# Optimization experiments

Measured on AMD Instinct MI355X. Metric: run time of the kernel, lower is better.

The kernel has to match this reference:

```python
import jax, jax.numpy as jnp
import numpy as np


def setup_inputs() -> dict:
    key = jax.random.key(0)
    k1, k2 = jax.random.split(key)
    B, D = 16384, 256
    return {
        "outputs": jax.random.normal(k1, (B, D), dtype=jnp.float32),
        "targets": jax.random.normal(k2, (B, D), dtype=jnp.float32),
    }


def reference(outputs, targets):
    # Cosine-similarity logits: (o @ t^T) / (||o||_row * ||t||_col)
    logits = outputs @ targets.T                      # [B, B]
    o_norm = jnp.linalg.norm(outputs, axis=1)         # [B]
    t_norm = jnp.linalg.norm(targets, axis=1)         # [B]
    logits = logits / o_norm[:, None] / t_norm[None, :]
    # Cross-entropy with labels = arange(B): mean over rows of (logsumexp - diag logit)
    logZ = jax.nn.logsumexp(logits, axis=1)           # [B]
    diag = jnp.diagonal(logits)                       # [B]
    loss = jnp.mean(logZ - diag)
    return loss
```

## Files before the change

kernel.cpp:

```cpp
#include <hip/hip_runtime.h>
#include <hip/hip_bf16.h>
#include <stdint.h>

#define BROWS 16384
#define DIM   256
#define BM    128
#define NBM   (BROWS / BM)
#define NBNR  16
#define NSTG  8
#define NCHUNK 32

#define LOG2E 1.44269504088896340736f

typedef __attribute__((ext_vector_type(8))) int  i32x8;
typedef __attribute__((ext_vector_type(4))) float f32x4;
typedef __attribute__((ext_vector_type(2))) float f32x2;
typedef unsigned char uchar;

#if __has_builtin(__builtin_amdgcn_exp2f)
#define EXP2(x) __builtin_amdgcn_exp2f(x)
#else
#define EXP2(x) exp2f(x)
#endif

__device__ __forceinline__ void gload_lds16(const void* g, void* l) {
  __builtin_amdgcn_global_load_lds(
      (const __attribute__((address_space(1))) void*)g,
      (__attribute__((address_space(3))) void*)l, 16, 0, 0);
}

__device__ __forceinline__ unsigned q4(float x) {
  float a = fabsf(x);
  unsigned q = (a >= 0.25f) + (a >= 0.75f) + (a >= 1.25f) + (a >= 1.75f) +
               (a >= 2.5f) + (a >= 3.5f) + (a >= 5.0f);
  return q | ((__float_as_uint(x) >> 28) & 8u);
}


__global__ void normalize_both(const float* __restrict__ o,
                               const float* __restrict__ t,
                               uchar* __restrict__ o4,
                               uchar* __restrict__ t4,
                               float* __restrict__ dlog) {
  int row  = blockIdx.x * 4 + (threadIdx.x >> 6);
  int lane = threadIdx.x & 63;
  float4 a = *(reinterpret_cast<const float4*>(o + (size_t)row * DIM) + lane);
  float4 b = *(reinterpret_cast<const float4*>(t + (size_t)row * DIM) + lane);
  float sso = a.x * a.x + a.y * a.y + a.z * a.z + a.w * a.w;
  float sst = b.x * b.x + b.y * b.y + b.z * b.z + b.w * b.w;
  float d   = a.x * b.x + a.y * b.y + a.z * b.z + a.w * b.w;
#pragma unroll
  for (int m = 1; m < 64; m <<= 1) {
    sso += __shfl_xor(sso, m);
    sst += __shfl_xor(sst, m);
    d   += __shfl_xor(d, m);
  }
  float ro = rsqrtf(sso);
  float rt = rsqrtf(sst);
  if (lane == 0) dlog[row] = d * ro * rt;
  float qo = ro * (16.0f * LOG2E);
  float qt = rt * 16.0f;
  unsigned wo = q4(a.x * qo) | (q4(a.y * qo) << 4) |
                (q4(a.z * qo) << 8) | (q4(a.w * qo) << 12);
  unsigned wt = q4(b.x * qt) | (q4(b.y * qt) << 4) |
                (q4(b.z * qt) << 8) | (q4(b.w * qt) << 12);
  size_t taddr = (size_t)(row >> 4) * 2048 + (size_t)((lane >> 3) * 256) +
                 (size_t)((row & 15) * 16) + (size_t)((lane & 7) * 2);
  *reinterpret_cast<unsigned short*>(o4 + taddr) = (unsigned short)wo;
  *reinterpret_cast<unsigned short*>(t4 + taddr) = (unsigned short)wt;
}

__global__ __launch_bounds__(512, 8) void gemm_expsum(
    const uchar* __restrict__ A4,
    const uchar* __restrict__ B4,
    float* __restrict__ partial) {
  __shared__ __align__(16) uchar Bs[2][16384];

  int b   = blockIdx.x;
  int xcd = b & 7;
  int idx = b >> 3;
  int bm  = xcd * 16 + (idx & 15);
  int bnr = idx >> 4;

  int tid  = threadIdx.x;
  int lane = tid & 63;
  int wid  = tid >> 6;
  int wr   = wid & 3;
  int wch  = wid >> 2;

  const uchar* Ap = A4 + (size_t)(bm * 8 + wr * 2) * 2048 + (size_t)lane * 16;
  const uchar* Bg = B4 + (size_t)bnr * 131072;

  i32x8 af[2][2];
#pragma unroll
  for (int m = 0; m < 2; ++m)
#pragma unroll
    for (int kt = 0; kt < 2; ++kt) {
      int4 d = *reinterpret_cast<const int4*>(Ap + m * 2048 + kt * 1024);
      af[m][kt] = (i32x8){d.x, d.y, d.z, d.w, 0, 0, 0, 0};
    }

  f32x2 v2[4];
#pragma unroll
  for (int j = 0; j < 4; ++j) v2[j] = (f32x2){0.f, 0.f};

  const f32x4 zero4 = {0.f, 0.f, 0.f, 0.f};
  i32x8 b0 = (i32x8){0, 0, 0, 0, 0, 0, 0, 0};
  i32x8 b1 = (i32x8){0, 0, 0, 0, 0, 0, 0, 0};

#define STAGE(st, s)                                                           \
  {                                                                            \
    _Pragma("unroll") for (int p = 0; p < 2; ++p)                              \
        gload_lds16(Bg + (size_t)(st) * 16384 + p * 8192 + wid * 1024 +        \
                        lane * 16,                                             \
                    (char*)Bs[s] + p * 8192 + wid * 1024 + lane * 16);         \
  }

#define COMPUTE(s)                                                             \
  {                                                                            \
    const uchar* bb = Bs[s];                                                   \
    _Pragma("unroll") for (int nn = 0; nn < 4; ++nn) {                         \
      const uchar* cb = bb + (wch * 4 + nn) * 2048 + lane * 16;                \
      *reinterpret_cast<int4*>(&b0) = *reinterpret_cast<const int4*>(cb);      \
      *reinterpret_cast<int4*>(&b1) = *reinterpret_cast<const int4*>(cb + 1024); \
      f32x4 a0 = __builtin_amdgcn_mfma_scale_f32_16x16x128_f8f6f4(             \
          af[0][0], b0, zero4, 4, 4, 0, 0x7B7B7B7B, 0, 0x7B7B7B7B);            \
      f32x4 a1 = __builtin_amdgcn_mfma_scale_f32_16x16x128_f8f6f4(             \
          af[1][0], b0, zero4, 4, 4, 0, 0x7B7B7B7B, 0, 0x7B7B7B7B);            \
      a0 = __builtin_amdgcn_mfma_scale_f32_16x16x128_f8f6f4(                   \
          af[0][1], b1, a0, 4, 4, 0, 0x7B7B7B7B, 0, 0x7B7B7B7B);               \
      a1 = __builtin_amdgcn_mfma_scale_f32_16x16x128_f8f6f4(                   \
          af[1][1], b1, a1, 4, 4, 0, 0x7B7B7B7B, 0, 0x7B7B7B7B);               \
      v2[0] += (f32x2){EXP2(a0[0]), EXP2(a0[1])};                              \
      v2[1] += (f32x2){EXP2(a0[2]), EXP2(a0[3])};                              \
      v2[2] += (f32x2){EXP2(a1[0]), EXP2(a1[1])};                              \
      v2[3] += (f32x2){EXP2(a1[2]), EXP2(a1[3])};                              \
    }                                                                          \
  }

  STAGE(0, 0);
  __syncthreads();
#pragma unroll
  for (int st = 0; st < NSTG; ++st) {
    if (st < NSTG - 1) STAGE(st + 1, (st + 1) & 1);
    COMPUTE(st & 1);
    if (st < NSTG - 1) __syncthreads();
  }
#undef STAGE
#undef COMPUTE

  float v[8];
#pragma unroll
  for (int j = 0; j < 8; ++j) v[j] = v2[j >> 1][j & 1];
#pragma unroll
  for (int s = 0; s < 3; ++s) {
    const int len = 8 >> s;
    const int bit = (lane >> s) & 1;
#pragma unroll
    for (int t = 0; t < 4; ++t) {
      if (t < (len >> 1)) {
        float a = v[2 * t], b2 = v[2 * t + 1];
        float recv = __shfl_xor(bit ? a : b2, 1 << s);
        v[t] = (bit ? b2 : a) + recv;
      }
    }
  }
  v[0] += __shfl_xor(v[0], 8);
  if ((lane & 8) == 0) {
    int j   = lane & 7;
    int sub = lane >> 4;
    int row = bm * BM + wr * 32 + (j >> 2) * 16 + sub * 4 + (j & 3);
    partial[(size_t)row * NCHUNK + ((bnr << 1) | wch)] = v[0];
  }
}

__global__ void row_finish(const float* __restrict__ partial,
                           const float* __restrict__ dlog,
                           float* __restrict__ rowloss) {
  int row = blockIdx.x * 256 + threadIdx.x;
  const float4* p = reinterpret_cast<const float4*>(partial + (size_t)row * NCHUNK);
  float s = 0.f;
#pragma unroll
  for (int q = 0; q < 8; ++q) {
    float4 pq = p[q];
    s += (pq.x + pq.y) + (pq.z + pq.w);
  }
  rowloss[row] = logf(s) - dlog[row];
}

__global__ void final_reduce(const float* __restrict__ rl, float* __restrict__ out) {
  __shared__ float sm[16];
  float s = 0.f;
  for (int i = threadIdx.x; i < BROWS; i += 1024) s += rl[i];
#pragma unroll
  for (int m = 1; m < 64; m <<= 1) s += __shfl_xor(s, m);
  int wid = threadIdx.x >> 6, lane = threadIdx.x & 63;
  if (lane == 0) sm[wid] = s;
  __syncthreads();
  if (wid == 0) {
    float v = (lane < 16) ? sm[lane] : 0.f;
#pragma unroll
    for (int m = 1; m < 16; m <<= 1) v += __shfl_xor(v, m);
    if (lane == 0) out[0] = v / (float)BROWS;
  }
}

extern "C" void kernel_launch(void* const* d_in, const int* in_sizes, int n_in,
                              void* d_out, int out_size, void* d_ws, size_t ws_size,
                              hipStream_t stream) {
  const float* outputs = (const float*)d_in[0];
  const float* targets = (const float*)d_in[1];
  float* out = (float*)d_out;
  char* ws = (char*)d_ws;

  uchar* o4      = (uchar*)ws;
  uchar* t4      = (uchar*)(ws + (size_t)2 * 1024 * 1024);
  float* partial = (float*)(ws + (size_t)4 * 1024 * 1024);
  float* dlog    = (float*)(ws + (size_t)6 * 1024 * 1024);
  float* rowloss = (float*)(ws + (size_t)6 * 1024 * 1024 + 65536);

  normalize_both<<<BROWS / 4, 256, 0, stream>>>(outputs, targets, o4, t4, dlog);
  gemm_expsum<<<NBM * NBNR, 512, 0, stream>>>(o4, t4, partial);
  row_finish<<<BROWS / 256, 256, 0, stream>>>(partial, dlog, rowloss);
  final_reduce<<<1, 1024, 0, stream>>>(rowloss, out);
}
```

Baseline: 63.16 us.

## Switch FP4 GEMM to 32x32x64 scaled MFMA with matching operand layout

Replaces the 16x16x128 FP4 scaled MFMA tiles with 32x32x64 tiles. The packed FP4 layout written by the normalize kernel changes to 32-row groups to match, and the warp tiling becomes 2 row-warps by 4 column-warps, each producing 64x32 outputs per stage. The larger MFMA is meant to give more work per instruction and fewer B-operand LDS reads per output. In exchange it needs more accumulator and exp registers (launch bounds drop to 4 blocks/SM), a longer shuffle reduction, and twice as many partial-sum columns for row_finish to read.

New measurement: 68.49 us. +8.4%, slower.

```diff
diff --git a/kernel.cpp b/kernel.cpp
--- a/kernel.cpp
+++ b/kernel.cpp
@@ -8,13 +8,12 @@
 #define NBM   (BROWS / BM)
 #define NBNR  16
 #define NSTG  8
-#define NCHUNK 32
+#define NCHUNK 64
 
 #define LOG2E 1.44269504088896340736f
 
-typedef __attribute__((ext_vector_type(8))) int  i32x8;
-typedef __attribute__((ext_vector_type(4))) float f32x4;
-typedef __attribute__((ext_vector_type(2))) float f32x2;
+typedef __attribute__((ext_vector_type(8)))  int   i32x8;
+typedef __attribute__((ext_vector_type(16))) float f32x16;
 typedef unsigned char uchar;
 
 #if __has_builtin(__builtin_amdgcn_exp2f)
@@ -64,13 +63,13 @@
                 (q4(a.z * qo) << 8) | (q4(a.w * qo) << 12);
   unsigned wt = q4(b.x * qt) | (q4(b.y * qt) << 4) |
                 (q4(b.z * qt) << 8) | (q4(b.w * qt) << 12);
-  size_t taddr = (size_t)(row >> 4) * 2048 + (size_t)((lane >> 3) * 256) +
-                 (size_t)((row & 15) * 16) + (size_t)((lane & 7) * 2);
-  *reinterpret_cast<unsigned short*>(o4 + taddr) = (unsigned short)wo;
-  *reinterpret_cast<unsigned short*>(t4 + taddr) = (unsigned short)wt;
-}
-
-__global__ __launch_bounds__(512, 8) void gemm_expsum(
+  size_t taddr = (size_t)(row >> 5) * 4096 + (size_t)((lane >> 2) * 512) +
+                 (size_t)((row & 31) * 16) + (size_t)((lane & 3) * 4);
+  *reinterpret_cast<unsigned*>(o4 + taddr) = wo;
+  *reinterpret_cast<unsigned*>(t4 + taddr) = wt;
+}
+
+__global__ __launch_bounds__(512, 4) void gemm_expsum(
     const uchar* __restrict__ A4,
     const uchar* __restrict__ B4,
     float* __restrict__ partial) {
@@ -85,28 +84,27 @@
   int tid  = threadIdx.x;
   int lane = tid & 63;
   int wid  = tid >> 6;
-  int wr   = wid & 3;
-  int wch  = wid >> 2;
-
-  const uchar* Ap = A4 + (size_t)(bm * 8 + wr * 2) * 2048 + (size_t)lane * 16;
+  int wr   = wid & 1;
+  int wc   = wid >> 1;
+
+  const uchar* Ap = A4 + (size_t)(bm * 4 + wr * 2) * 4096 + (size_t)lane * 16;
   const uchar* Bg = B4 + (size_t)bnr * 131072;
 
-  i32x8 af[2][2];
-#pragma unroll
-  for (int m = 0; m < 2; ++m)
-#pragma unroll
-    for (int kt = 0; kt < 2; ++kt) {
-      int4 d = *reinterpret_cast<const int4*>(Ap + m * 2048 + kt * 1024);
-      af[m][kt] = (i32x8){d.x, d.y, d.z, d.w, 0, 0, 0, 0};
+  i32x8 af[2][4];
+#pragma unroll
+  for (int rt = 0; rt < 2; ++rt)
+#pragma unroll
+    for (int kt = 0; kt < 4; ++kt) {
+      int4 d = *reinterpret_cast<const int4*>(Ap + rt * 4096 + kt * 1024);
+      af[rt][kt] = (i32x8){d.x, d.y, d.z, d.w, 0, 0, 0, 0};
     }
 
-  f32x2 v2[4];
-#pragma unroll
-  for (int j = 0; j < 4; ++j) v2[j] = (f32x2){0.f, 0.f};
-
-  const f32x4 zero4 = {0.f, 0.f, 0.f, 0.f};
-  i32x8 b0 = (i32x8){0, 0, 0, 0, 0, 0, 0, 0};
-  i32x8 b1 = (i32x8){0, 0, 0, 0, 0, 0, 0, 0};
+  float v[32];
+#pragma unroll
+  for (int j = 0; j < 32; ++j) v[j] = 0.f;
+
+  const f32x16 zero16 = {0.f, 0.f, 0.f, 0.f, 0.f, 0.f, 0.f, 0.f,
+                         0.f, 0.f, 0.f, 0.f, 0.f, 0.f, 0.f, 0.f};
 
 #define STAGE(st, s)                                                           \
   {                                                                            \
@@ -118,23 +116,20 @@
 
 #define COMPUTE(s)                                                             \
   {                                                                            \
-    const uchar* bb = Bs[s];                                                   \
-    _Pragma("unroll") for (int nn = 0; nn < 4; ++nn) {                         \
-      const uchar* cb = bb + (wch * 4 + nn) * 2048 + lane * 16;                \
-      *reinterpret_cast<int4*>(&b0) = *reinterpret_cast<const int4*>(cb);      \
-      *reinterpret_cast<int4*>(&b1) = *reinterpret_cast<const int4*>(cb + 1024); \
-      f32x4 a0 = __builtin_amdgcn_mfma_scale_f32_16x16x128_f8f6f4(             \
-          af[0][0], b0, zero4, 4, 4, 0, 0x7B7B7B7B, 0, 0x7B7B7B7B);            \
-      f32x4 a1 = __builtin_amdgcn_mfma_scale_f32_16x16x128_f8f6f4(             \
-          af[1][0], b0, zero4, 4, 4, 0, 0x7B7B7B7B, 0, 0x7B7B7B7B);            \
-      a0 = __builtin_amdgcn_mfma_scale_f32_16x16x128_f8f6f4(                   \
-          af[0][1], b1, a0, 4, 4, 0, 0x7B7B7B7B, 0, 0x7B7B7B7B);               \
-      a1 = __builtin_amdgcn_mfma_scale_f32_16x16x128_f8f6f4(                   \
-          af[1][1], b1, a1, 4, 4, 0, 0x7B7B7B7B, 0, 0x7B7B7B7B);               \
-      v2[0] += (f32x2){EXP2(a0[0]), EXP2(a0[1])};                              \
-      v2[1] += (f32x2){EXP2(a0[2]), EXP2(a0[3])};                              \
-      v2[2] += (f32x2){EXP2(a1[0]), EXP2(a1[1])};                              \
-      v2[3] += (f32x2){EXP2(a1[2]), EXP2(a1[3])};                              \
+    const uchar* bb = Bs[s] + wc * 4096 + lane * 16;                           \
+    f32x16 a0 = zero16, a1 = zero16;                                           \
+    _Pragma("unroll") for (int kt = 0; kt < 4; ++kt) {                         \
+      i32x8 bf = (i32x8){0, 0, 0, 0, 0, 0, 0, 0};                              \
+      *reinterpret_cast<int4*>(&bf) =                                          \
+          *reinterpret_cast<const int4*>(bb + kt * 1024);                      \
+      a0 = __builtin_amdgcn_mfma_scale_f32_32x32x64_f8f6f4(                    \
+          af[0][kt], bf, a0, 4, 4, 0, 0x7B7B7B7B, 0, 0x7B7B7B7B);              \
+      a1 = __builtin_amdgcn_mfma_scale_f32_32x32x64_f8f6f4(                    \
+          af[1][kt], bf, a1, 4, 4, 0, 0x7B7B7B7B, 0, 0x7B7B7B7B);              \
+    }                                                                          \
+    _Pragma("unroll") for (int r = 0; r < 16; ++r) {                           \
+      v[r]      += EXP2(a0[r]);                                                \
+      v[16 + r] += EXP2(a1[r]);                                                \
     }                                                                          \
   }
 
@@ -149,15 +144,12 @@
 #undef STAGE
 #undef COMPUTE
 
-  float v[8];
-#pragma unroll
-  for (int j = 0; j < 8; ++j) v[j] = v2[j >> 1][j & 1];
-#pragma unroll
-  for (int s = 0; s < 3; ++s) {
-    const int len = 8 >> s;
+#pragma unroll
+  for (int s = 0; s < 5; ++s) {
+    const int len = 32 >> s;
     const int bit = (lane >> s) & 1;
 #pragma unroll
-    for (int t = 0; t < 4; ++t) {
+    for (int t = 0; t < 16; ++t) {
       if (t < (len >> 1)) {
         float a = v[2 * t], b2 = v[2 * t + 1];
         float recv = __shfl_xor(bit ? a : b2, 1 << s);
@@ -165,12 +157,12 @@
       }
     }
   }
-  v[0] += __shfl_xor(v[0], 8);
-  if ((lane & 8) == 0) {
-    int j   = lane & 7;
-    int sub = lane >> 4;
-    int row = bm * BM + wr * 32 + (j >> 2) * 16 + sub * 4 + (j & 3);
-    partial[(size_t)row * NCHUNK + ((bnr << 1) | wch)] = v[0];
+  {
+    int j   = lane & 31;
+    int reg = j & 15;
+    int row = bm * BM + wr * 64 + (j >> 4) * 32 +
+              (reg & 3) + 8 * (reg >> 2) + 4 * (lane >> 5);
+    partial[(size_t)row * NCHUNK + ((bnr << 2) | wc)] = v[0];
   }
 }
 
@@ -181,7 +173,7 @@
   const float4* p = reinterpret_cast<const float4*>(partial + (size_t)row * NCHUNK);
   float s = 0.f;
 #pragma unroll
-  for (int q = 0; q < 8; ++q) {
+  for (int q = 0; q < 16; ++q) {
     float4 pq = p[q];
     s += (pq.x + pq.y) + (pq.z + pq.w);
   }
@@ -216,8 +208,8 @@
   uchar* o4      = (uchar*)ws;
   uchar* t4      = (uchar*)(ws + (size_t)2 * 1024 * 1024);
   float* partial = (float*)(ws + (size_t)4 * 1024 * 1024);
-  float* dlog    = (float*)(ws + (size_t)6 * 1024 * 1024);
-  float* rowloss = (float*)(ws + (size_t)6 * 1024 * 1024 + 65536);
+  float* dlog    = (float*)(ws + (size_t)8 * 1024 * 1024);
+  float* rowloss = (float*)(ws + (size_t)8 * 1024 * 1024 + 65536);
 
   normalize_both<<<BROWS / 4, 256, 0, stream>>>(outputs, targets, o4, t4, dlog);
   gemm_expsum<<<NBM * NBNR, 512, 0, stream>>>(o4, t4, partial);
```
